# Kernel tuning notes

Hardware: AMD Instinct MI355X
Metric: run time of the kernel (lower is better)

The kernel has to match this reference:

```python
import jax, jax.numpy as jnp
import numpy as np

DIM = 1024
LATENT_DIM = 512
NUM_HEADS = 16
HEAD_DIM = DIM // NUM_HEADS
SCALE = HEAD_DIM ** -0.5


def setup_inputs() -> dict:
    key = jax.random.key(0)
    k1, k2, k3, k4, k5 = jax.random.split(key, 5)
    B, xN, zN = 2, 2048, 2048
    x = jax.random.normal(k1, (B, xN, DIM), dtype=jnp.float32)
    z = jax.random.normal(k2, (B, zN, LATENT_DIM), dtype=jnp.float32)
    # torch Linear weights: [out_features, in_features]
    Wq = jax.random.normal(k3, (DIM, DIM), dtype=jnp.float32) * (DIM ** -0.5)
    Wkv = jax.random.normal(k4, (2 * DIM, LATENT_DIM), dtype=jnp.float32) * (LATENT_DIM ** -0.5)
    Wo = jax.random.normal(k5, (DIM, DIM), dtype=jnp.float32) * (DIM ** -0.5)
    return {"x": x, "z": z, "Wq": Wq, "Wkv": Wkv, "Wo": Wo}


def reference(x, z, Wq, Wkv, Wo):
    B, xN, _ = x.shape
    _, zN, _ = z.shape
    # projections (torch Linear: y = x @ W.T)
    Q = (x @ Wq.T).reshape(B, xN, NUM_HEADS, HEAD_DIM)        # [B,xN,H,D]
    KV = (z @ Wkv.T).reshape(B, zN, 2, NUM_HEADS, HEAD_DIM)   # [B,zN,2,H,D]
    K = KV[:, :, 0]                                            # [B,zN,H,D]
    V = KV[:, :, 1]
    attn = jnp.einsum('bqhd,bkhd->bhqk', Q, K) * SCALE         # [B,H,xN,zN]
    attn = jax.nn.softmax(attn, axis=-1)
    O = jnp.einsum('bhqk,bkhd->bqhd', attn, V).reshape(B, xN, DIM)
    return O @ Wo.T
```

## Files before the change

kernel.cpp:

```cpp
#include <hip/hip_runtime.h>
#include <stdint.h>

#define SEQ 2048
#define QSCALE 0.1803368801111244f
#define DEFER_THR 11.5f

typedef __attribute__((ext_vector_type(8))) short bf16x8;
typedef __attribute__((ext_vector_type(4))) short bf16x4;
typedef __attribute__((ext_vector_type(4))) float f32x4;
typedef __attribute__((ext_vector_type(16))) float f32x16;
typedef unsigned short u16;

__device__ __forceinline__ u16 f2bf(float f) {
  union { float f; uint32_t u; } v; v.f = f;
  uint32_t u = v.u;
  u += 0x7fffu + ((u >> 16) & 1u);
  return (u16)(u >> 16);
}

__device__ __forceinline__ float fast_exp2(float x) {
#if __has_builtin(__builtin_amdgcn_exp2f)
  return __builtin_amdgcn_exp2f(x);
#else
  return exp2f(x);
#endif
}

__device__ __forceinline__ uint32_t cvtpk(float a, float b) {
  uint32_t r;
  asm("v_cvt_pk_bf16_f32 %0, %1, %2" : "=v"(r) : "v"(a), "v"(b));
  return r;
}

__device__ __forceinline__ void swap_pair(uint32_t& a, uint32_t& b, int hi) {
  uint32_t ta = (uint32_t)__shfl_xor((int)a, 32);
  uint32_t tb = (uint32_t)__shfl_xor((int)b, 32);
  a = hi ? tb : a;
  b = hi ? b : ta;
}

__device__ __forceinline__ void gload_lds16(const u16* g, u16* l) {
  __builtin_amdgcn_global_load_lds((__attribute__((address_space(1))) void*)g,
                                   (__attribute__((address_space(3))) void*)l,
                                   16, 0, 0);
}

__global__ void cvt5_kernel(const float* __restrict__ x, const float* __restrict__ z,
                            const float* __restrict__ Wq, const float* __restrict__ Wkv,
                            const float* __restrict__ Wo,
                            u16* __restrict__ xb, u16* __restrict__ zb,
                            u16* __restrict__ wqb, u16* __restrict__ wkvb,
                            u16* __restrict__ wob) {
  const int X4 = 1048576, Z4 = 524288, W4 = 262144;
  const int total = X4 + Z4 + 3 * W4;
  int i = blockIdx.x * blockDim.x + threadIdx.x;
  const int stride = gridDim.x * blockDim.x;
  for (; i < total; i += stride) {
    const float* src; u16* dst; int j = i;
    if (j < X4)              { src = x;   dst = xb; }
    else if ((j -= X4) < Z4) { src = z;   dst = zb; }
    else if ((j -= Z4) < W4) { src = Wq;  dst = wqb; }
    else if ((j -= W4) < W4) { src = Wkv; dst = wkvb; }
    else       { j -= W4;      src = Wo;  dst = wob; }
    float4 v = ((const float4*)src)[j];
    bf16x4 o;
    o[0] = (short)f2bf(v.x); o[1] = (short)f2bf(v.y);
    o[2] = (short)f2bf(v.z); o[3] = (short)f2bf(v.w);
    ((bf16x4*)dst)[j] = o;
  }
}

template <int BN, typename CT>
__device__ __forceinline__ void gemm_bt_body(const u16* __restrict__ A,
                                             const u16* __restrict__ B,
                                             CT* __restrict__ C,
                                             int N, int K, float scale,
                                             int tm, int tn, u16* As, u16* Bs) {
  constexpr int NB = BN / 32;
  constexpr int NBG = BN / 64;
  const int tid = threadIdx.x;
  const int wid = tid >> 6;
  const int lane = tid & 63;
  const int lg = lane >> 4, lq = lane & 15;
  const int wr = wid >> 1, wc = wid & 1;

  f32x4 acc[4][NB];
#pragma unroll
  for (int m = 0; m < 4; m++)
#pragma unroll
    for (int n = 0; n < NB; n++)
#pragma unroll
      for (int e = 0; e < 4; e++) acc[m][n][e] = 0.f;

  const int r0 = tid >> 2;
  const int s0 = tid & 3;
  const int sc = (s0 ^ ((r0 >> 1) & 3)) * 8;
  const u16* gA0 = A + (size_t)(tm * 128 + r0) * K + sc;
  const u16* gA1 = gA0 + (size_t)64 * K;
  const u16* gB0 = B + (size_t)(tn * BN + r0) * K + sc;
  const u16* gB1 = gB0 + (size_t)64 * K;
  u16* lA = As + wid * 512;
  u16* lB = Bs + wid * 512;

  const int rslot = (lg ^ ((lq >> 1) & 3)) * 8;

  for (int k0 = 0; k0 < K; k0 += 32) {
    __syncthreads();
    gload_lds16(gA0 + k0, lA);
    gload_lds16(gA1 + k0, lA + 2048);
    gload_lds16(gB0 + k0, lB);
    if constexpr (NBG == 2) gload_lds16(gB1 + k0, lB + 2048);
    __syncthreads();

    bf16x8 af[4], bfr[NB];
#pragma unroll
    for (int m = 0; m < 4; m++)
      af[m] = *(const bf16x8*)(As + (wr * 64 + m * 16 + lq) * 32 + rslot);
#pragma unroll
    for (int n = 0; n < NB; n++)
      bfr[n] = *(const bf16x8*)(Bs + (wc * (BN / 2) + n * 16 + lq) * 32 + rslot);
#pragma unroll
    for (int m = 0; m < 4; m++)
#pragma unroll
      for (int n = 0; n < NB; n++)
        acc[m][n] = __builtin_amdgcn_mfma_f32_16x16x32_bf16(af[m], bfr[n], acc[m][n], 0, 0, 0);
  }

#pragma unroll
  for (int m = 0; m < 4; m++) {
    const int row = tm * 128 + wr * 64 + m * 16 + lg * 4;
#pragma unroll
    for (int i = 0; i < 4; i++) {
      CT* cp = C + (size_t)(row + i) * N + tn * BN + wc * (BN / 2) + lq;
#pragma unroll
      for (int n = 0; n < NB; n++) {
        float v = acc[m][n][i] * scale;
        if constexpr (sizeof(CT) == 2) cp[n * 16] = (CT)f2bf(v);
        else                            cp[n * 16] = (CT)v;
      }
    }
  }
}

__global__ __launch_bounds__(256) void qkv_gemm(const u16* __restrict__ xb,
                                                const u16* __restrict__ zb,
                                                const u16* __restrict__ Wqb,
                                                const u16* __restrict__ Wkvb,
                                                u16* __restrict__ Qb,
                                                u16* __restrict__ Kb,
                                                u16* __restrict__ VTb) {
  __shared__ __align__(16) u16 As[128 * 32];
  __shared__ __align__(16) u16 Bs[128 * 32];
  int g = blockIdx.x;
  if (g < 256) {
    gemm_bt_body<128, u16>(xb, Wqb, Qb, 1024, 1024, QSCALE, g >> 3, g & 7, As, Bs);
  } else if (g < 512) {
    g -= 256;
    gemm_bt_body<128, u16>(zb, Wkvb, Kb, 1024, 512, 1.f, g >> 3, g & 7, As, Bs);
  } else {
    g -= 512;
    gemm_bt_body<128, u16>(Wkvb + 1024 * 512, zb, VTb, 4096, 512, 1.f, g >> 5, g & 31, As, Bs);
  }
}

__global__ __launch_bounds__(256) void o_gemm(const u16* __restrict__ Ob,
                                              const u16* __restrict__ Wob,
                                              float* __restrict__ out) {
  __shared__ __align__(16) u16 As[128 * 32];
  __shared__ __align__(16) u16 Bs[64 * 32];
  gemm_bt_body<64, float>(Ob, Wob, out, 1024, 1024, 1.f, blockIdx.y, blockIdx.x, As, Bs);
}

__global__ __launch_bounds__(256, 4) void attn_kernel(const u16* __restrict__ Q,
                                                      const u16* __restrict__ K,
                                                      const u16* __restrict__ VT,
                                                      u16* __restrict__ OP,
                                                      float2* __restrict__ ml) {
  __shared__ __align__(16) u16 LDS[16384];

  const int tid = threadIdx.x;
  const int wid = tid >> 6;
  const int lane = tid & 63;
  const int l31 = lane & 31;
  const int hi = lane >> 5;

  const int bi = blockIdx.x;
  const int xcd = bi & 7, j = bi >> 3;
  const int qt = j & 15;
  const int s  = (j >> 4) & 1;
  const int bh = xcd + 8 * (j >> 5);
  const int b = bh >> 4, h = bh & 15;
  const int t0 = s * 16;

  const int q0 = qt * 128 + wid * 32;

  bf16x8 qf[4];
  {
    const u16* qp = Q + (size_t)(b * SEQ + q0 + l31) * 1024 + h * 64 + hi * 8;
#pragma unroll
    for (int ks = 0; ks < 4; ks++) qf[ks] = *(const bf16x8*)(qp + ks * 16);
  }

  f32x16 of[2];
#pragma unroll
  for (int d = 0; d < 2; d++)
#pragma unroll
    for (int e = 0; e < 16; e++) of[d][e] = 0.f;
  float m_run = -3.0e38f, l_run = 0.f;

  const char* rdB[4];
#pragma unroll
  for (int ks = 0; ks < 4; ks++)
    rdB[ks] = (const char*)LDS + l31 * 128 + ((((2 * ks + hi) ^ (lane & 7))) << 4);

  const int r0 = tid >> 3;
  const int srcc = ((tid & 7) ^ (r0 & 7)) << 3;
  const u16* gK = K + (size_t)(b * SEQ + r0) * 1024 + h * 64 + srcc;
  const u16* gV = VT + (size_t)(h * 64 + r0) * 4096 + b * SEQ + srcc;
  u16* lK = LDS + wid * 512;
  u16* lV = LDS + 8192 + wid * 512;

  auto stage = [&](int t, int buf) {
    const u16* sk = gK + (size_t)t * 64 * 1024;
    gload_lds16(sk, lK + buf * 4096);
    gload_lds16(sk + (size_t)32 * 1024, lK + buf * 4096 + 2048);
    const u16* sv = gV + t * 64;
    gload_lds16(sv, lV + buf * 4096);
    gload_lds16(sv + (size_t)32 * 4096, lV + buf * 4096 + 2048);
  };

  auto tile_compute = [&](int buf) {
    const int bo = buf * 8192;

    f32x16 sacc[2];
#pragma unroll
    for (int kb = 0; kb < 2; kb++)
#pragma unroll
      for (int e = 0; e < 16; e++) sacc[kb][e] = 0.f;
    __builtin_amdgcn_s_setprio(1);
#pragma unroll
    for (int kb = 0; kb < 2; kb++)
#pragma unroll
      for (int ks = 0; ks < 4; ks++) {
        bf16x8 kf = *(const bf16x8*)(rdB[ks] + bo + kb * 4096);
        sacc[kb] = __builtin_amdgcn_mfma_f32_32x32x16_bf16(kf, qf[ks], sacc[kb], 0, 0, 0);
      }
    __builtin_amdgcn_s_setprio(0);

    float a0 = sacc[0][0], a1 = sacc[0][1], a2 = sacc[0][2], a3 = sacc[0][3];
#pragma unroll
    for (int e = 4; e < 16; e += 4) {
      a0 = fmaxf(a0, sacc[0][e]);     a1 = fmaxf(a1, sacc[0][e + 1]);
      a2 = fmaxf(a2, sacc[0][e + 2]); a3 = fmaxf(a3, sacc[0][e + 3]);
    }
#pragma unroll
    for (int e = 0; e < 16; e += 4) {
      a0 = fmaxf(a0, sacc[1][e]);     a1 = fmaxf(a1, sacc[1][e + 1]);
      a2 = fmaxf(a2, sacc[1][e + 2]); a3 = fmaxf(a3, sacc[1][e + 3]);
    }
    float tmax = fmaxf(fmaxf(a0, a1), fmaxf(a2, a3));
    tmax = fmaxf(tmax, __shfl_xor(tmax, 32));

    if (!__all(tmax <= m_run + DEFER_THR)) {
      const float m_new = fmaxf(m_run, tmax);
      const float esc = fast_exp2(m_run - m_new);
      l_run *= esc;
#pragma unroll
      for (int r = 0; r < 16; r++) {
        const int qof = (r & 3) + 8 * (r >> 2) + 4 * hi;
        const float e = __shfl(esc, qof);
        of[0][r] *= e;
        of[1][r] *= e;
      }
      m_run = m_new;
    }

    float s0 = 0.f, s1 = 0.f, s2 = 0.f, s3 = 0.f;
#pragma unroll
    for (int kb = 0; kb < 2; kb++)
#pragma unroll
      for (int e = 0; e < 16; e += 4) {
        float p0 = fast_exp2(sacc[kb][e] - m_run);
        float p1 = fast_exp2(sacc[kb][e + 1] - m_run);
        float p2 = fast_exp2(sacc[kb][e + 2] - m_run);
        float p3 = fast_exp2(sacc[kb][e + 3] - m_run);
        sacc[kb][e] = p0; sacc[kb][e + 1] = p1; sacc[kb][e + 2] = p2; sacc[kb][e + 3] = p3;
        s0 += p0; s1 += p1; s2 += p2; s3 += p3;
      }
    l_run += (s0 + s1) + (s2 + s3);

    bf16x8 pa[4];
#pragma unroll
    for (int kb = 0; kb < 2; kb++) {
      uint32_t c0 = cvtpk(sacc[kb][0],  sacc[kb][1]);
      uint32_t c1 = cvtpk(sacc[kb][2],  sacc[kb][3]);
      uint32_t c2 = cvtpk(sacc[kb][4],  sacc[kb][5]);
      uint32_t c3 = cvtpk(sacc[kb][6],  sacc[kb][7]);
      uint32_t c4 = cvtpk(sacc[kb][8],  sacc[kb][9]);
      uint32_t c5 = cvtpk(sacc[kb][10], sacc[kb][11]);
      uint32_t c6 = cvtpk(sacc[kb][12], sacc[kb][13]);
      uint32_t c7 = cvtpk(sacc[kb][14], sacc[kb][15]);
      swap_pair(c0, c2, hi);
      swap_pair(c1, c3, hi);
      swap_pair(c4, c6, hi);
      swap_pair(c5, c7, hi);
      union { bf16x8 v; uint32_t d[4]; } u0, u1;
      u0.d[0] = c0; u0.d[1] = c1; u0.d[2] = c2; u0.d[3] = c3;
      u1.d[0] = c4; u1.d[1] = c5; u1.d[2] = c6; u1.d[3] = c7;
      pa[2 * kb] = u0.v;
      pa[2 * kb + 1] = u1.v;
    }

    __builtin_amdgcn_s_setprio(1);
#pragma unroll
    for (int ks = 0; ks < 4; ks++)
#pragma unroll
      for (int db = 0; db < 2; db++) {
        bf16x8 vf = *(const bf16x8*)(rdB[ks] + bo + 16384 + db * 4096);
        of[db] = __builtin_amdgcn_mfma_f32_32x32x16_bf16(pa[ks], vf, of[db], 0, 0, 0);
      }
    __builtin_amdgcn_s_setprio(0);
  };

  stage(t0, 0);
  __syncthreads();
#pragma unroll 1
  for (int tt = 0; tt < 16; tt += 2) {
    stage(t0 + tt + 1, 1);
    tile_compute(0);
    __syncthreads();
    if (tt < 14) stage(t0 + tt + 2, 0);
    tile_compute(1);
    __syncthreads();
  }

  const float lsum = l_run + __shfl_xor(l_run, 32);
  const float linv = 1.f / lsum;

  u16* OPs = OP + (size_t)s * 4096 * 1024;
#pragma unroll
  for (int r = 0; r < 16; r++) {
    const int qof = (r & 3) + 8 * (r >> 2) + 4 * hi;
    const float li = __shfl(linv, qof);
    u16* op = OPs + (size_t)(b * SEQ + q0 + qof) * 1024 + h * 64 + l31;
    op[0]  = f2bf(of[0][r] * li);
    op[32] = f2bf(of[1][r] * li);
  }
  if (hi == 0) {
    const int grow = b * SEQ + q0 + l31;
    ml[s * (4096 * 16) + grow * 16 + h] = make_float2(m_run, lsum);
  }
}

__global__ __launch_bounds__(256) void combine_kernel(const u16* __restrict__ OP,
                                                      const float2* __restrict__ ml,
                                                      u16* __restrict__ Ob) {
  const int i = blockIdx.x * 256 + threadIdx.x;
  const int grow = i >> 7;
  const int h = (i >> 3) & 15;
  const float2 a0 = ml[grow * 16 + h];
  const float2 a1 = ml[4096 * 16 + grow * 16 + h];
  const float M = fmaxf(a0.x, a1.x);
  float w0 = a0.y * fast_exp2(a0.x - M);
  float w1 = a1.y * fast_exp2(a1.x - M);
  const float inv = 1.f / (w0 + w1);
  w0 *= inv; w1 *= inv;
  const bf16x8 p0 = ((const bf16x8*)OP)[i];
  const bf16x8 p1 = ((const bf16x8*)(OP + (size_t)4096 * 1024))[i];
  bf16x8 o;
#pragma unroll
  for (int e = 0; e < 8; e++) {
    union { uint32_t u; float f; } f0, f1;
    f0.u = ((uint32_t)(u16)p0[e]) << 16;
    f1.u = ((uint32_t)(u16)p1[e]) << 16;
    o[e] = (short)f2bf(w0 * f0.f + w1 * f1.f);
  }
  ((bf16x8*)Ob)[i] = o;
}

extern "C" void kernel_launch(void* const* d_in, const int* in_sizes, int n_in,
                              void* d_out, int out_size, void* d_ws, size_t ws_size,
                              hipStream_t stream) {
  const float* x   = (const float*)d_in[0];
  const float* z   = (const float*)d_in[1];
  const float* Wq  = (const float*)d_in[2];
  const float* Wkv = (const float*)d_in[3];
  const float* Wo  = (const float*)d_in[4];
  float* out = (float*)d_out;

  char* ws = (char*)d_ws;
  const size_t MB = 1024ull * 1024ull;
  u16* xb   = (u16*)(ws + 0);
  u16* zb   = (u16*)(ws + 8 * MB);
  u16* Wqb  = (u16*)(ws + 12 * MB);
  u16* Wkvb = (u16*)(ws + 14 * MB);
  u16* Wob  = (u16*)(ws + 16 * MB);
  u16* Qb   = (u16*)(ws + 18 * MB);
  u16* Kb   = (u16*)(ws + 26 * MB);
  u16* VTb  = (u16*)(ws + 34 * MB);
  u16* Ob   = (u16*)(ws + 42 * MB);
  u16* OP   = (u16*)(ws + 0);
  float2* ml = (float2*)(ws + 50 * MB);

  cvt5_kernel<<<2048, 256, 0, stream>>>(x, z, Wq, Wkv, Wo, xb, zb, Wqb, Wkvb, Wob);

  qkv_gemm<<<768, 256, 0, stream>>>(xb, zb, Wqb, Wkvb, Qb, Kb, VTb);

  attn_kernel<<<1024, 256, 0, stream>>>(Qb, Kb, VTb, OP, ml);

  combine_kernel<<<2048, 256, 0, stream>>>(OP, ml, Ob);

  o_gemm<<<dim3(16, 32), 256, 0, stream>>>(Ob, Wob, out);
}
```

Measured before the change: 121.8 us.

## Fuse split-KV combine into output GEMM, widen QKV GEMM K-tile, hoist V loads

Removes the separate combine kernel by merging the two split-KV partial outputs (log-sum-exp weights) directly in the output projection GEMM's A-tile staging, which avoids writing and re-reading the intermediate O buffer and saves one launch. The QKV GEMM now uses a 64-wide K step with an 8-slot XOR swizzle and a 3-block occupancy hint. In the attention kernel, V fragments are loaded from LDS before the softmax so their latency can overlap the exp math. In exchange, the fused GEMM recomputes the combine weights for every N-tile, reads OP redundantly across 16 column blocks, and stages A through registers instead of direct global-to-LDS loads.

```diff
diff --git a/kernel.cpp b/kernel.cpp
--- a/kernel.cpp
+++ b/kernel.cpp
@@ -16,6 +16,12 @@
   uint32_t u = v.u;
   u += 0x7fffu + ((u >> 16) & 1u);
   return (u16)(u >> 16);
+}
+
+__device__ __forceinline__ float bf2f(u16 b) {
+  union { uint32_t u; float f; } v;
+  v.u = ((uint32_t)b) << 16;
+  return v.f;
 }
 
 __device__ __forceinline__ float fast_exp2(float x) {
@@ -70,59 +76,178 @@
   }
 }
 
-template <int BN, typename CT>
-__device__ __forceinline__ void gemm_bt_body(const u16* __restrict__ A,
-                                             const u16* __restrict__ B,
-                                             CT* __restrict__ C,
-                                             int N, int K, float scale,
-                                             int tm, int tn, u16* As, u16* Bs) {
-  constexpr int NB = BN / 32;
-  constexpr int NBG = BN / 64;
+__device__ __forceinline__ void gemm64_body(const u16* __restrict__ A,
+                                            const u16* __restrict__ B,
+                                            u16* __restrict__ C,
+                                            int N, int K, float scale,
+                                            int tm, int tn, u16* As, u16* Bs) {
   const int tid = threadIdx.x;
   const int wid = tid >> 6;
   const int lane = tid & 63;
   const int lg = lane >> 4, lq = lane & 15;
   const int wr = wid >> 1, wc = wid & 1;
 
-  f32x4 acc[4][NB];
+  f32x4 acc[4][4];
 #pragma unroll
   for (int m = 0; m < 4; m++)
 #pragma unroll
-    for (int n = 0; n < NB; n++)
+    for (int n = 0; n < 4; n++)
 #pragma unroll
       for (int e = 0; e < 4; e++) acc[m][n][e] = 0.f;
 
-  const int r0 = tid >> 2;
-  const int s0 = tid & 3;
-  const int sc = (s0 ^ ((r0 >> 1) & 3)) * 8;
-  const u16* gA0 = A + (size_t)(tm * 128 + r0) * K + sc;
-  const u16* gA1 = gA0 + (size_t)64 * K;
-  const u16* gB0 = B + (size_t)(tn * BN + r0) * K + sc;
-  const u16* gB1 = gB0 + (size_t)64 * K;
+  const int r0 = tid >> 3;
+  const int c0 = tid & 7;
+  const int sc = (c0 ^ (r0 & 7)) * 8;
+  const u16* gA = A + (size_t)(tm * 128 + r0) * K + sc;
+  const u16* gB = B + (size_t)(tn * 128 + r0) * K + sc;
   u16* lA = As + wid * 512;
   u16* lB = Bs + wid * 512;
 
+  for (int k0 = 0; k0 < K; k0 += 64) {
+    __syncthreads();
+#pragma unroll
+    for (int i = 0; i < 4; i++) {
+      gload_lds16(gA + k0 + (size_t)(32 * i) * K, lA + i * 2048);
+      gload_lds16(gB + k0 + (size_t)(32 * i) * K, lB + i * 2048);
+    }
+    __syncthreads();
+
+#pragma unroll
+    for (int ks = 0; ks < 2; ks++) {
+      const int slot = ((ks * 4 + lg) ^ (lq & 7)) * 8;
+      bf16x8 af[4], bfr[4];
+#pragma unroll
+      for (int m = 0; m < 4; m++)
+        af[m] = *(const bf16x8*)(As + (wr * 64 + m * 16 + lq) * 64 + slot);
+#pragma unroll
+      for (int n = 0; n < 4; n++)
+        bfr[n] = *(const bf16x8*)(Bs + (wc * 64 + n * 16 + lq) * 64 + slot);
+#pragma unroll
+      for (int m = 0; m < 4; m++)
+#pragma unroll
+        for (int n = 0; n < 4; n++)
+          acc[m][n] = __builtin_amdgcn_mfma_f32_16x16x32_bf16(af[m], bfr[n], acc[m][n], 0, 0, 0);
+    }
+  }
+
+#pragma unroll
+  for (int m = 0; m < 4; m++) {
+    const int row = tm * 128 + wr * 64 + m * 16 + lg * 4;
+#pragma unroll
+    for (int i = 0; i < 4; i++) {
+      u16* cp = C + (size_t)(row + i) * N + tn * 128 + wc * 64 + lq;
+#pragma unroll
+      for (int n = 0; n < 4; n++)
+        cp[n * 16] = f2bf(acc[m][n][i] * scale);
+    }
+  }
+}
+
+__global__ __launch_bounds__(256, 3) void qkv_gemm(const u16* __restrict__ xb,
+                                                   const u16* __restrict__ zb,
+                                                   const u16* __restrict__ Wqb,
+                                                   const u16* __restrict__ Wkvb,
+                                                   u16* __restrict__ Qb,
+                                                   u16* __restrict__ Kb,
+                                                   u16* __restrict__ VTb) {
+  __shared__ __align__(16) u16 As[128 * 64];
+  __shared__ __align__(16) u16 Bs[128 * 64];
+  int g = blockIdx.x;
+  if (g < 256) {
+    gemm64_body(xb, Wqb, Qb, 1024, 1024, QSCALE, g >> 3, g & 7, As, Bs);
+  } else if (g < 512) {
+    g -= 256;
+    gemm64_body(zb, Wkvb, Kb, 1024, 512, 1.f, g >> 3, g & 7, As, Bs);
+  } else {
+    g -= 512;
+    gemm64_body(Wkvb + 1024 * 512, zb, VTb, 4096, 512, 1.f, g >> 5, g & 31, As, Bs);
+  }
+}
+
+__global__ __launch_bounds__(256) void o_gemm_combine(const u16* __restrict__ OP,
+                                                      const float2* __restrict__ ml,
+                                                      const u16* __restrict__ Wob,
+                                                      float* __restrict__ out) {
+  __shared__ __align__(16) u16 As[128 * 32];
+  __shared__ __align__(16) u16 Bs[64 * 32];
+  const int tid = threadIdx.x;
+  const int wid = tid >> 6;
+  const int lane = tid & 63;
+  const int lg = lane >> 4, lq = lane & 15;
+  const int wr = wid >> 1, wc = wid & 1;
+  const int tm = blockIdx.y, tn = blockIdx.x;
+
+  f32x4 acc[4][2];
+#pragma unroll
+  for (int m = 0; m < 4; m++)
+#pragma unroll
+    for (int n = 0; n < 2; n++)
+#pragma unroll
+      for (int e = 0; e < 4; e++) acc[m][n][e] = 0.f;
+
+  const int r0 = tid >> 2;
+  const int c0 = tid & 3;
+  const int slotA = c0 ^ ((r0 >> 1) & 3);
+  const int grow0 = tm * 128 + r0;
+
+  const u16* gO00 = OP + (size_t)grow0 * 1024;
+  const u16* gO01 = gO00 + (size_t)4096 * 1024;
+  const u16* gO10 = gO00 + (size_t)64 * 1024;
+  const u16* gO11 = gO01 + (size_t)64 * 1024;
+  const float2* mlr0 = ml + (size_t)grow0 * 16;
+  const float2* mlr1 = mlr0 + 64 * 16;
+
+  const u16* gB = Wob + (size_t)(tn * 64 + r0) * 1024 + slotA * 8;
+  u16* lB = Bs + wid * 512;
+
   const int rslot = (lg ^ ((lq >> 1) & 3)) * 8;
 
-  for (int k0 = 0; k0 < K; k0 += 32) {
-    __syncthreads();
-    gload_lds16(gA0 + k0, lA);
-    gload_lds16(gA1 + k0, lA + 2048);
-    gload_lds16(gB0 + k0, lB);
-    if constexpr (NBG == 2) gload_lds16(gB1 + k0, lB + 2048);
-    __syncthreads();
-
-    bf16x8 af[4], bfr[NB];
+  for (int k0 = 0; k0 < 1024; k0 += 32) {
+    const int col = k0 + c0 * 8;
+    const int h = k0 >> 6;
+    __syncthreads();
+    bf16x8 p00 = *(const bf16x8*)(gO00 + col);
+    bf16x8 p01 = *(const bf16x8*)(gO01 + col);
+    bf16x8 p10 = *(const bf16x8*)(gO10 + col);
+    bf16x8 p11 = *(const bf16x8*)(gO11 + col);
+    const float2 a0 = mlr0[h], b0 = mlr0[65536 + h];
+    const float2 a1 = mlr1[h], b1 = mlr1[65536 + h];
+    gload_lds16(gB + k0, lB);
+
+    float M0 = fmaxf(a0.x, b0.x);
+    float w00 = a0.y * fast_exp2(a0.x - M0);
+    float w01 = b0.y * fast_exp2(b0.x - M0);
+    float i0 = 1.f / (w00 + w01); w00 *= i0; w01 *= i0;
+    float M1 = fmaxf(a1.x, b1.x);
+    float w10 = a1.y * fast_exp2(a1.x - M1);
+    float w11 = b1.y * fast_exp2(b1.x - M1);
+    float i1 = 1.f / (w10 + w11); w10 *= i1; w11 *= i1;
+
+    union { bf16x8 v; uint32_t d[4]; } A0, A1;
+#pragma unroll
+    for (int e = 0; e < 8; e += 2) {
+      float f0 = w00 * bf2f((u16)p00[e])     + w01 * bf2f((u16)p01[e]);
+      float f1 = w00 * bf2f((u16)p00[e + 1]) + w01 * bf2f((u16)p01[e + 1]);
+      A0.d[e >> 1] = cvtpk(f0, f1);
+      float g0 = w10 * bf2f((u16)p10[e])     + w11 * bf2f((u16)p11[e]);
+      float g1 = w10 * bf2f((u16)p10[e + 1]) + w11 * bf2f((u16)p11[e + 1]);
+      A1.d[e >> 1] = cvtpk(g0, g1);
+    }
+    *(bf16x8*)(As + r0 * 32 + slotA * 8) = A0.v;
+    *(bf16x8*)(As + (r0 + 64) * 32 + slotA * 8) = A1.v;
+    __syncthreads();
+
+    bf16x8 af[4], bfr[2];
 #pragma unroll
     for (int m = 0; m < 4; m++)
       af[m] = *(const bf16x8*)(As + (wr * 64 + m * 16 + lq) * 32 + rslot);
 #pragma unroll
-    for (int n = 0; n < NB; n++)
-      bfr[n] = *(const bf16x8*)(Bs + (wc * (BN / 2) + n * 16 + lq) * 32 + rslot);
+    for (int n = 0; n < 2; n++)
+      bfr[n] = *(const bf16x8*)(Bs + (wc * 32 + n * 16 + lq) * 32 + rslot);
 #pragma unroll
     for (int m = 0; m < 4; m++)
 #pragma unroll
-      for (int n = 0; n < NB; n++)
+      for (int n = 0; n < 2; n++)
         acc[m][n] = __builtin_amdgcn_mfma_f32_16x16x32_bf16(af[m], bfr[n], acc[m][n], 0, 0, 0);
   }
 
@@ -131,44 +256,11 @@
     const int row = tm * 128 + wr * 64 + m * 16 + lg * 4;
 #pragma unroll
     for (int i = 0; i < 4; i++) {
-      CT* cp = C + (size_t)(row + i) * N + tn * BN + wc * (BN / 2) + lq;
-#pragma unroll
-      for (int n = 0; n < NB; n++) {
-        float v = acc[m][n][i] * scale;
-        if constexpr (sizeof(CT) == 2) cp[n * 16] = (CT)f2bf(v);
-        else                            cp[n * 16] = (CT)v;
-      }
-    }
-  }
-}
-
-__global__ __launch_bounds__(256) void qkv_gemm(const u16* __restrict__ xb,
-                                                const u16* __restrict__ zb,
-                                                const u16* __restrict__ Wqb,
-                                                const u16* __restrict__ Wkvb,
-                                                u16* __restrict__ Qb,
-                                                u16* __restrict__ Kb,
-                                                u16* __restrict__ VTb) {
-  __shared__ __align__(16) u16 As[128 * 32];
-  __shared__ __align__(16) u16 Bs[128 * 32];
-  int g = blockIdx.x;
-  if (g < 256) {
-    gemm_bt_body<128, u16>(xb, Wqb, Qb, 1024, 1024, QSCALE, g >> 3, g & 7, As, Bs);
-  } else if (g < 512) {
-    g -= 256;
-    gemm_bt_body<128, u16>(zb, Wkvb, Kb, 1024, 512, 1.f, g >> 3, g & 7, As, Bs);
-  } else {
-    g -= 512;
-    gemm_bt_body<128, u16>(Wkvb + 1024 * 512, zb, VTb, 4096, 512, 1.f, g >> 5, g & 31, As, Bs);
-  }
-}
-
-__global__ __launch_bounds__(256) void o_gemm(const u16* __restrict__ Ob,
-                                              const u16* __restrict__ Wob,
-                                              float* __restrict__ out) {
-  __shared__ __align__(16) u16 As[128 * 32];
-  __shared__ __align__(16) u16 Bs[64 * 32];
-  gemm_bt_body<64, float>(Ob, Wob, out, 1024, 1024, 1.f, blockIdx.y, blockIdx.x, As, Bs);
+      float* cp = out + (size_t)(row + i) * 1024 + tn * 64 + wc * 32 + lq;
+#pragma unroll
+      for (int n = 0; n < 2; n++) cp[n * 16] = acc[m][n][i];
+    }
+  }
 }
 
 __global__ __launch_bounds__(256, 4) void attn_kernel(const u16* __restrict__ Q,
@@ -246,6 +338,13 @@
         sacc[kb] = __builtin_amdgcn_mfma_f32_32x32x16_bf16(kf, qf[ks], sacc[kb], 0, 0, 0);
       }
     __builtin_amdgcn_s_setprio(0);
+
+    bf16x8 vf0[4], vf1[4];
+#pragma unroll
+    for (int ks = 0; ks < 4; ks++) {
+      vf0[ks] = *(const bf16x8*)(rdB[ks] + bo + 16384);
+      vf1[ks] = *(const bf16x8*)(rdB[ks] + bo + 16384 + 4096);
+    }
 
     float a0 = sacc[0][0], a1 = sacc[0][1], a2 = sacc[0][2], a3 = sacc[0][3];
 #pragma unroll
@@ -313,12 +412,10 @@
 
     __builtin_amdgcn_s_setprio(1);
 #pragma unroll
-    for (int ks = 0; ks < 4; ks++)
-#pragma unroll
-      for (int db = 0; db < 2; db++) {
-        bf16x8 vf = *(const bf16x8*)(rdB[ks] + bo + 16384 + db * 4096);
-        of[db] = __builtin_amdgcn_mfma_f32_32x32x16_bf16(pa[ks], vf, of[db], 0, 0, 0);
-      }
+    for (int ks = 0; ks < 4; ks++) {
+      of[0] = __builtin_amdgcn_mfma_f32_32x32x16_bf16(pa[ks], vf0[ks], of[0], 0, 0, 0);
+      of[1] = __builtin_amdgcn_mfma_f32_32x32x16_bf16(pa[ks], vf1[ks], of[1], 0, 0, 0);
+    }
     __builtin_amdgcn_s_setprio(0);
   };
 
@@ -350,32 +447,6 @@
     const int grow = b * SEQ + q0 + l31;
     ml[s * (4096 * 16) + grow * 16 + h] = make_float2(m_run, lsum);
   }
-}
-
-__global__ __launch_bounds__(256) void combine_kernel(const u16* __restrict__ OP,
-                                                      const float2* __restrict__ ml,
-                                                      u16* __restrict__ Ob) {
-  const int i = blockIdx.x * 256 + threadIdx.x;
-  const int grow = i >> 7;
-  const int h = (i >> 3) & 15;
-  const float2 a0 = ml[grow * 16 + h];
-  const float2 a1 = ml[4096 * 16 + grow * 16 + h];
-  const float M = fmaxf(a0.x, a1.x);
-  float w0 = a0.y * fast_exp2(a0.x - M);
-  float w1 = a1.y * fast_exp2(a1.x - M);
-  const float inv = 1.f / (w0 + w1);
-  w0 *= inv; w1 *= inv;
-  const bf16x8 p0 = ((const bf16x8*)OP)[i];
-  const bf16x8 p1 = ((const bf16x8*)(OP + (size_t)4096 * 1024))[i];
-  bf16x8 o;
-#pragma unroll
-  for (int e = 0; e < 8; e++) {
-    union { uint32_t u; float f; } f0, f1;
-    f0.u = ((uint32_t)(u16)p0[e]) << 16;
-    f1.u = ((uint32_t)(u16)p1[e]) << 16;
-    o[e] = (short)f2bf(w0 * f0.f + w1 * f1.f);
-  }
-  ((bf16x8*)Ob)[i] = o;
 }
 
 extern "C" void kernel_launch(void* const* d_in, const int* in_sizes, int n_in,
@@ -398,7 +469,6 @@
   u16* Qb   = (u16*)(ws + 18 * MB);
   u16* Kb   = (u16*)(ws + 26 * MB);
   u16* VTb  = (u16*)(ws + 34 * MB);
-  u16* Ob   = (u16*)(ws + 42 * MB);
   u16* OP   = (u16*)(ws + 0);
   float2* ml = (float2*)(ws + 50 * MB);
 
@@ -408,7 +478,5 @@
 
   attn_kernel<<<1024, 256, 0, stream>>>(Qb, Kb, VTb, OP, ml);
 
-  combine_kernel<<<2048, 256, 0, stream>>>(OP, ml, Ob);
-
-  o_gemm<<<dim3(16, 32), 256, 0, stream>>>(Ob, Wob, out);
-}
+  o_gemm_combine<<<dim3(16, 32), 256, 0, stream>>>(OP, ml, Wob, out);
+}
```

After: 163.5 us. 34.2% more time.
